# Optimization experiments

Hardware: AMD Instinct MI355X
Metric: run time of the kernel (lower is better)

Reference implementation:

```python
import jax, jax.numpy as jnp
import numpy as np

N = 20000          # nodes
E = 320000         # edges (avg degree 16)
MUL = 64           # multiplicity of 0e and 1o in hidden irreps
NUM_BASIS = 8
HID = 64           # radial MLP hidden
NSPEC = 4          # node attribute (species) scalars
N_NEIGH = 16.0
SILU_NORM = 1.679177  # e3nn normalize2mom constant for silu


def silu_n(x):
    return jax.nn.silu(x) * SILU_NORM


def setup_inputs() -> dict:
    key = jax.random.key(0)
    ks = jax.random.split(key, 20)
    inp = {
        'node_scalars': jax.random.normal(ks[0], (N, MUL), jnp.float32),
        'node_vectors': jax.random.normal(ks[1], (N, MUL, 3), jnp.float32),
        'node_attr': jax.random.uniform(ks[2], (N, NSPEC), jnp.float32),
        'edge_sh': jax.random.normal(ks[3], (E, 4), jnp.float32),
        'edge_embedded': jax.random.uniform(ks[4], (E, NUM_BASIS), jnp.float32),
        'edge_src': jax.random.randint(ks[5], (E,), 0, N),
        'edge_dst': jax.random.randint(ks[6], (E,), 0, N),
        # e3nn Linear #1 (64x0e+64x1o -> same)
        'W_lin1_s': jax.random.normal(ks[7], (MUL, MUL), jnp.float32),
        'W_lin1_v': jax.random.normal(ks[8], (MUL, MUL), jnp.float32),
        # radial FullyConnectedNet 8 -> 64 -> 64 -> 256
        'W_fc0': jax.random.normal(ks[9], (NUM_BASIS, HID), jnp.float32),
        'W_fc1': jax.random.normal(ks[10], (HID, HID), jnp.float32),
        'W_fc2': jax.random.normal(ks[11], (HID, 4 * MUL), jnp.float32),
        # e3nn Linear #2 (128x0e+128x1o -> 128x0e+64x1o)
        'W_lin2_s': jax.random.normal(ks[12], (2 * MUL, 2 * MUL), jnp.float32),
        'W_lin2_v': jax.random.normal(ks[13], (2 * MUL, MUL), jnp.float32),
        # self-connection FullyConnectedTensorProduct weights
        'W_sc_s': jax.random.normal(ks[14], (MUL, NSPEC, 2 * MUL), jnp.float32),
        'W_sc_v': jax.random.normal(ks[15], (MUL, NSPEC, MUL), jnp.float32),
    }
    return inp


def reference(node_scalars, node_vectors, node_attr, edge_sh, edge_embedded,
              W_lin1_s, W_lin1_v, W_fc0, W_fc1, W_fc2, W_lin2_s, W_lin2_v,
              W_sc_s, W_sc_v, edge_src, edge_dst):
    inv_sqrt3 = 1.0 / jnp.sqrt(jnp.float32(3.0))
    # ---- self connection (FullyConnectedTensorProduct with scalar attrs) ----
    sc_norm = 1.0 / jnp.sqrt(jnp.float32(MUL * NSPEC))
    sc_s = jnp.einsum('nu,nv,uvw->nw', node_scalars, node_attr, W_sc_s) * sc_norm   # [N,128]
    sc_v = jnp.einsum('nui,nv,uvw->nwi', node_vectors, node_attr, W_sc_v) * sc_norm  # [N,64,3]
    # ---- e3nn Linear #1 ----
    lin_norm = 1.0 / jnp.sqrt(jnp.float32(MUL))
    s = (node_scalars @ W_lin1_s) * lin_norm                      # [N,64]
    v = jnp.einsum('nui,uw->nwi', node_vectors, W_lin1_v) * lin_norm  # [N,64,3]
    # ---- gather to edges ----
    s_e = s[edge_src]          # [E,64]
    v_e = v[edge_src]          # [E,64,3]
    y0 = edge_sh[:, :1]        # [E,1]  (0e)
    y1 = edge_sh[:, 1:4]       # [E,3]  (1o)
    # ---- radial MLP -> per-edge TP weights ----
    h = silu_n((edge_embedded @ W_fc0) / jnp.sqrt(jnp.float32(NUM_BASIS)))
    h = silu_n((h @ W_fc1) / jnp.sqrt(jnp.float32(HID)))
    w = (h @ W_fc2) / jnp.sqrt(jnp.float32(HID))                  # [E,256]
    wA, wB, wC, wD = w[:, :MUL], w[:, MUL:2*MUL], w[:, 2*MUL:3*MUL], w[:, 3*MUL:]
    # ---- per-edge CG tensor product ('uvu', component normalization) ----
    oA = wA * s_e * y0                                            # 0e x 0e -> 0e  [E,64]
    oD = wD * jnp.einsum('eui,ei->eu', v_e, y1) * inv_sqrt3       # 1o x 1o -> 0e  [E,64]
    oB = wB[:, :, None] * s_e[:, :, None] * y1[:, None, :]        # 0e x 1o -> 1o  [E,64,3]
    oC = wC[:, :, None] * v_e * y0[:, :, None]                    # 1o x 0e -> 1o  [E,64,3]
    # ---- scatter-sum to destination nodes, normalize by neighbors ----
    s_agg = jax.ops.segment_sum(jnp.concatenate([oA, oD], axis=-1), edge_dst, num_segments=N) / N_NEIGH  # [N,128]
    v_agg = jax.ops.segment_sum(jnp.concatenate([oB, oC], axis=1), edge_dst, num_segments=N) / N_NEIGH   # [N,128,3]
    # ---- e3nn Linear #2 (128x0e+128x1o -> 128x0e+64x1o) ----
    lin2_norm = 1.0 / jnp.sqrt(jnp.float32(2 * MUL))
    s_h = (s_agg @ W_lin2_s) * lin2_norm                          # [N,128]
    v_h = jnp.einsum('nui,uw->nwi', v_agg, W_lin2_v) * lin2_norm  # [N,64,3]
    # ---- self connection ----
    s_h = s_h + sc_s
    v_h = v_h + sc_v
    # ---- Gate (even irreps -> normalized silu) ----
    out_s = silu_n(s_h[:, :MUL])                                  # scalars [N,64]
    out_v = silu_n(s_h[:, MUL:])[:, :, None] * v_h                # gated vectors [N,64,3]
    return jnp.concatenate([out_s, out_v.reshape(out_v.shape[0], MUL * 3)], axis=-1)  # [N,256]
```

## Files before the change

### kernel.cpp

```cpp
#include <hip/hip_runtime.h>
#include <math.h>

#define N_NODES 20000
#define N_EDGES 320000
#define MUL 64
#define NUM_BASIS 8
#define HID 64
#define NSPEC 4

#define LIN_NORM     0.125f
#define INV_SQRT8    0.3535533906f
#define LIN2_NORM    0.08838834765f
#define SC_NORM      0.0625f
#define INV_NEIGH    0.0625f
#define INV_SQRT3    0.5773502692f
#define SILU_NORM    1.679177f

typedef __attribute__((ext_vector_type(8))) short bf16x8;
typedef __attribute__((ext_vector_type(4))) float f32x4;

__device__ __forceinline__ float silu_n(float x) {
    float s = 1.0f / (1.0f + __expf(-x));
    return x * s * SILU_NORM;
}

__device__ __forceinline__ float bcast(float x, int l) {
    return __uint_as_float(__builtin_amdgcn_readlane(__float_as_uint(x), l));
}
__device__ __forceinline__ int bcast_i(int x, int l) {
    return __builtin_amdgcn_readlane(x, l);
}

__device__ __forceinline__ unsigned short f2bf(float x) {
    unsigned int u = __float_as_uint(x);
    unsigned int r = (u + 0x7fffu + ((u >> 16) & 1u)) >> 16;
    return (unsigned short)r;
}

__device__ __forceinline__ unsigned int cvtpk(float lo, float hi) {
    unsigned int r;
    asm("v_cvt_pk_bf16_f32 %0, %1, %2" : "=v"(r) : "v"(lo), "v"(hi));
    return r;
}

__device__ __forceinline__ bf16x8 cvt8(float f0, float f1, float f2, float f3,
                                       float f4, float f5, float f6, float f7) {
    union { unsigned int u[4]; bf16x8 v; } r;
    r.u[0] = cvtpk(f0, f1);
    r.u[1] = cvtpk(f2, f3);
    r.u[2] = cvtpk(f4, f5);
    r.u[3] = cvtpk(f6, f7);
    return r.v;
}

__global__ __launch_bounds__(256) void k_hist(const int* __restrict__ edst,
                                              int* __restrict__ counts)
{
    int e = blockIdx.x * blockDim.x + threadIdx.x;
    if (e < N_EDGES) atomicAdd(&counts[edst[e]], 1);
}

#define SCAN_T 1024
__global__ __launch_bounds__(SCAN_T) void k_scan(const int* __restrict__ counts,
                                                 int* __restrict__ cursor)
{
    __shared__ int part[SCAN_T];
    int t = threadIdx.x;
    const int CH = (N_NODES + SCAN_T - 1) / SCAN_T;
    int b0 = t * CH;
    int s = 0;
    for (int i = 0; i < CH; ++i) {
        int idx = b0 + i;
        if (idx < N_NODES) s += counts[idx];
    }
    part[t] = s;
    __syncthreads();
    for (int off = 1; off < SCAN_T; off <<= 1) {
        int v = (t >= off) ? part[t - off] : 0;
        __syncthreads();
        part[t] += v;
        __syncthreads();
    }
    int run = (t == 0) ? 0 : part[t - 1];
    for (int i = 0; i < CH; ++i) {
        int idx = b0 + i;
        if (idx < N_NODES) {
            cursor[idx] = run;
            run += counts[idx];
        }
    }
}

__global__ __launch_bounds__(256) void k_fill(const int* __restrict__ edst,
                                              const int* __restrict__ esrc,
                                              const float* __restrict__ sh,
                                              const float* __restrict__ emb,
                                              int* __restrict__ cursor,
                                              int* __restrict__ dlist,
                                              int* __restrict__ slist,
                                              float4* __restrict__ ysort,
                                              float4* __restrict__ esort)
{
    int e = blockIdx.x * blockDim.x + threadIdx.x;
    if (e < N_EDGES) {
        int d = edst[e];
        int pos = atomicAdd(&cursor[d], 1);
        dlist[pos] = d;
        slist[pos] = esrc[e];
        ysort[pos] = ((const float4*)sh)[e];
        esort[(size_t)pos * 2]     = ((const float4*)emb)[(size_t)e * 2];
        esort[(size_t)pos * 2 + 1] = ((const float4*)emb)[(size_t)e * 2 + 1];
    }
}

__global__ __launch_bounds__(256) void k_wprep(
    const float* __restrict__ W1, const float* __restrict__ W2,
    const float* __restrict__ Wl2s, const float* __restrict__ Wl2v,
    const float* __restrict__ Wscs, const float* __restrict__ Wscv,
    const float* __restrict__ W0,
    const float* __restrict__ Wl1s, const float* __restrict__ Wl1v,
    unsigned short* __restrict__ w1f, unsigned short* __restrict__ w2f,
    unsigned short* __restrict__ bsf, unsigned short* __restrict__ bvf,
    unsigned short* __restrict__ w0f,
    unsigned short* __restrict__ l1sf, unsigned short* __restrict__ l1vf)
{
    int t = blockIdx.x * 256 + threadIdx.x;
    if (t < 512) {
        int f = t >> 6, lane = t & 63;
        int kt = f >> 2, nt = f & 3, q = lane >> 4, c = lane & 15;
        #pragma unroll
        for (int j = 0; j < 8; ++j) {
            int k = kt * 32 + q * 8 + j;
            int n = nt * 16 + c;
            w1f[(size_t)t * 8 + j] = f2bf(W1[k * 64 + n]);
        }
    } else if (t < 2560) {
        int tt = t - 512;
        int f = tt >> 6, lane = tt & 63;
        int kt = f >> 4, nt = f & 15, q = lane >> 4, c = lane & 15;
        #pragma unroll
        for (int j = 0; j < 8; ++j) {
            int k = kt * 32 + q * 8 + j;
            int n = nt * 16 + c;
            w2f[(size_t)tt * 8 + j] = f2bf(W2[k * 256 + n]);
        }
    } else if (t < 4608) {
        int tt = t - 2560;
        int f = tt >> 6, lane = tt & 63;
        int kt = f >> 3, nt = f & 7, q = lane >> 4, c = lane & 15;
        #pragma unroll
        for (int j = 0; j < 8; ++j) {
            int k = kt * 32 + q * 8 + j;
            int n = nt * 16 + c;
            bsf[(size_t)tt * 8 + j] = f2bf(Wl2s[k * 128 + n] * LIN2_NORM);
        }
    } else if (t < 8704) {
        int tt = t - 4608;
        int f = tt >> 6, lane = tt & 63;
        int v = f >> 4, g = f & 15;
        int kt = g >> 3, nt = g & 7, q = lane >> 4, c = lane & 15;
        #pragma unroll
        for (int j = 0; j < 8; ++j) {
            int u = kt * 32 + q * 8 + j;
            int n = nt * 16 + c;
            bsf[(size_t)(2048 + tt) * 8 + j] = f2bf(Wscs[(u * 4 + v) * 128 + n] * SC_NORM);
        }
    } else if (t < 9728) {
        int tt = t - 8704;
        int f = tt >> 6, lane = tt & 63;
        int kt = f >> 2, nt = f & 3, q = lane >> 4, c = lane & 15;
        #pragma unroll
        for (int j = 0; j < 8; ++j) {
            int k = kt * 32 + q * 8 + j;
            int n = nt * 16 + c;
            bvf[(size_t)tt * 8 + j] = f2bf(Wl2v[k * 64 + n] * LIN2_NORM);
        }
    } else if (t < 11776) {
        int tt = t - 9728;
        int f = tt >> 6, lane = tt & 63;
        int v = f >> 3, g = f & 7;
        int kt = g >> 2, nt = g & 3, q = lane >> 4, c = lane & 15;
        #pragma unroll
        for (int j = 0; j < 8; ++j) {
            int u = kt * 32 + q * 8 + j;
            int n = nt * 16 + c;
            bvf[(size_t)(1024 + tt) * 8 + j] = f2bf(Wscv[(u * 4 + v) * 64 + n] * SC_NORM);
        }
    } else if (t < 12032) {
        int tt = t - 11776;
        int f = tt >> 6, lane = tt & 63;
        int q = lane >> 4, c = lane & 15;
        #pragma unroll
        for (int j = 0; j < 8; ++j) {
            int k = q * 8 + j;
            int n = f * 16 + c;
            w0f[(size_t)tt * 8 + j] =
                (k < 8) ? f2bf(W0[k * 64 + n] * INV_SQRT8) : (unsigned short)0;
        }
    } else if (t < 12544) {
        int tt = t - 12032;
        int f = tt >> 6, lane = tt & 63;
        int kt = f >> 2, nt = f & 3, q = lane >> 4, c = lane & 15;
        #pragma unroll
        for (int j = 0; j < 8; ++j) {
            int k = kt * 32 + q * 8 + j;
            int n = nt * 16 + c;
            l1sf[(size_t)tt * 8 + j] = f2bf(Wl1s[k * 64 + n] * LIN_NORM);
        }
    } else if (t < 13056) {
        int tt = t - 12544;
        int f = tt >> 6, lane = tt & 63;
        int kt = f >> 2, nt = f & 3, q = lane >> 4, c = lane & 15;
        #pragma unroll
        for (int j = 0; j < 8; ++j) {
            int k = kt * 32 + q * 8 + j;
            int n = nt * 16 + c;
            l1vf[(size_t)tt * 8 + j] = f2bf(Wl1v[k * 64 + n] * LIN_NORM);
        }
    }
}

__global__ __launch_bounds__(256) void k_node_lin1(
    const float* __restrict__ ns, const float* __restrict__ nv,
    const unsigned short* __restrict__ l1sf, const unsigned short* __restrict__ l1vf,
    float* __restrict__ s_out, float* __restrict__ v_out)
{
    const size_t NV = (size_t)N_NODES * 64;
    int lane = threadIdx.x & 63;
    int wtile = (blockIdx.x * blockDim.x + threadIdx.x) >> 6;
    int n0 = __builtin_amdgcn_readfirstlane(wtile * 16);
    if (n0 >= N_NODES) return;
    int q = lane >> 4, c = lane & 15;
    int node = n0 + c;

    f32x4 Ds[4];
    #pragma unroll
    for (int nt = 0; nt < 4; ++nt) Ds[nt] = (f32x4){0.f, 0.f, 0.f, 0.f};
    #pragma unroll
    for (int kt = 0; kt < 2; ++kt) {
        const float* ap = ns + (size_t)node * 64 + kt * 32 + q * 8;
        float4 a0 = *(const float4*)ap;
        float4 a1 = *(const float4*)(ap + 4);
        bf16x8 A = cvt8(a0.x, a0.y, a0.z, a0.w, a1.x, a1.y, a1.z, a1.w);
        #pragma unroll
        for (int nt = 0; nt < 4; ++nt) {
            bf16x8 B = *(const bf16x8*)(l1sf + (size_t)((kt * 4 + nt) * 64 + lane) * 8);
            Ds[nt] = __builtin_amdgcn_mfma_f32_16x16x32_bf16(A, B, Ds[nt], 0, 0, 0);
        }
    }
    #pragma unroll
    for (int nt = 0; nt < 4; ++nt)
        #pragma unroll
        for (int r = 0; r < 4; ++r)
            s_out[(size_t)(n0 + q * 4 + r) * 64 + nt * 16 + c] = Ds[nt][r];

    #pragma unroll 1
    for (int p = 0; p < 3; ++p) {
        f32x4 Dv[4];
        #pragma unroll
        for (int nt = 0; nt < 4; ++nt) Dv[nt] = (f32x4){0.f, 0.f, 0.f, 0.f};
        #pragma unroll
        for (int kt = 0; kt < 2; ++kt) {
            float f[8];
            #pragma unroll
            for (int j = 0; j < 8; ++j)
                f[j] = nv[(size_t)node * 192 + (size_t)(kt * 32 + q * 8 + j) * 3 + p];
            bf16x8 A = cvt8(f[0], f[1], f[2], f[3], f[4], f[5], f[6], f[7]);
            #pragma unroll
            for (int nt = 0; nt < 4; ++nt) {
                bf16x8 B = *(const bf16x8*)(l1vf + (size_t)((kt * 4 + nt) * 64 + lane) * 8);
                Dv[nt] = __builtin_amdgcn_mfma_f32_16x16x32_bf16(A, B, Dv[nt], 0, 0, 0);
            }
        }
        #pragma unroll
        for (int nt = 0; nt < 4; ++nt)
            #pragma unroll
            for (int r = 0; r < 4; ++r)
                v_out[p * NV + (size_t)(n0 + q * 4 + r) * 64 + nt * 16 + c] = Dv[nt][r];
    }
}

__global__ __launch_bounds__(256) void k_edge_fused(
    const float* __restrict__ esort,
    const unsigned short* __restrict__ w0f,
    const unsigned short* __restrict__ w1f, const unsigned short* __restrict__ w2f,
    const int* __restrict__ slist, const int* __restrict__ dlist,
    const float* __restrict__ ysort,
    const float* __restrict__ s_in, const float* __restrict__ v_in,
    float* __restrict__ s_agg, float* __restrict__ v_agg)
{
    const size_t NP2 = (size_t)N_NODES * 128;
    const size_t NV  = (size_t)N_NODES * 64;

    __shared__ unsigned short h0t[4 * 16 * 72];
    __shared__ unsigned short h1t[4 * 16 * 72];
    __shared__ unsigned int   wl1[4 * 16 * 66];
    __shared__ unsigned int   wl2[4 * 16 * 66];

    int lane = threadIdx.x & 63;
    int wid  = threadIdx.x >> 6;
    int q = lane >> 4;
    int c = lane & 15;
    int lbase = __builtin_amdgcn_readfirstlane(blockIdx.x * 256 + wid * 64);
    unsigned short* myh0 = h0t + wid * (16 * 72);
    unsigned short* myh1 = h1t + wid * (16 * 72);
    unsigned int*   myw1 = wl1 + wid * (16 * 66);
    unsigned int*   myw2 = wl2 + wid * (16 * 66);

    int srcv = slist[lbase + lane];
    int dstv = dlist[lbase + lane];
    float4 y4 = ((const float4*)ysort)[lbase + lane];

    bf16x8 B0[4];
    #pragma unroll
    for (int f = 0; f < 4; ++f)
        B0[f] = *(const bf16x8*)(w0f + (size_t)(f * 64 + lane) * 8);
    bf16x8 B1[2][4];
    #pragma unroll
    for (int f = 0; f < 8; ++f)
        B1[f >> 2][f & 3] = *(const bf16x8*)(w1f + (size_t)(f * 64 + lane) * 8);

    const float4* e4 = (const float4*)esort;
    const float WS  = 0.125f * INV_NEIGH;
    const float WSD = WS * INV_SQRT3;

    float accA = 0.f, aB0 = 0.f, aB1 = 0.f, aB2 = 0.f;
    float accD = 0.f, aC0 = 0.f, aC1 = 0.f, aC2 = 0.f;
    int cur = bcast_i(dstv, 0);

    #pragma unroll 1
    for (int mt = 0; mt < 4; ++mt) {
        int tb16 = mt * 16;

        float4 ea = {0.f, 0.f, 0.f, 0.f}, eb = {0.f, 0.f, 0.f, 0.f};
        if (q == 0) {
            ea = e4[(size_t)(lbase + tb16 + c) * 2];
            eb = e4[(size_t)(lbase + tb16 + c) * 2 + 1];
        }
        bf16x8 Ae = cvt8(ea.x, ea.y, ea.z, ea.w, eb.x, eb.y, eb.z, eb.w);
        f32x4 D0[4];
        #pragma unroll
        for (int nt = 0; nt < 4; ++nt) {
            f32x4 z = {0.f, 0.f, 0.f, 0.f};
            D0[nt] = __builtin_amdgcn_mfma_f32_16x16x32_bf16(Ae, B0[nt], z, 0, 0, 0);
        }
        #pragma unroll
        for (int nt = 0; nt < 4; ++nt)
            #pragma unroll
            for (int r = 0; r < 4; ++r)
                myh0[(q * 4 + r) * 72 + nt * 16 + c] = f2bf(silu_n(D0[nt][r]));
        __builtin_amdgcn_s_waitcnt(0xC07F);
        bf16x8 A0[2];
        #pragma unroll
        for (int kt = 0; kt < 2; ++kt)
            A0[kt] = *(const bf16x8*)(myh0 + c * 72 + kt * 32 + q * 8);

        f32x4 D1[4];
        #pragma unroll
        for (int nt = 0; nt < 4; ++nt) {
            f32x4 z = {0.f, 0.f, 0.f, 0.f};
            D1[nt] = __builtin_amdgcn_mfma_f32_16x16x32_bf16(A0[0], B1[0][nt], z, 0, 0, 0);
            D1[nt] = __builtin_amdgcn_mfma_f32_16x16x32_bf16(A0[1], B1[1][nt], D1[nt], 0, 0, 0);
        }
        #pragma unroll
        for (int nt = 0; nt < 4; ++nt)
            #pragma unroll
            for (int r = 0; r < 4; ++r)
                myh1[(q * 4 + r) * 72 + nt * 16 + c] = f2bf(silu_n(D1[nt][r] * 0.125f));
        __builtin_amdgcn_s_waitcnt(0xC07F);
        bf16x8 A1[2];
        #pragma unroll
        for (int kt = 0; kt < 2; ++kt)
            A1[kt] = *(const bf16x8*)(myh1 + c * 72 + kt * 32 + q * 8);

        #pragma unroll
        for (int half = 0; half < 2; ++half) {
            int ga = half * 2, gb = half * 2 + 1;
            f32x4 Da[4], Db[4];
            #pragma unroll
            for (int ntl = 0; ntl < 4; ++ntl) {
                bf16x8 b0 = *(const bf16x8*)(w2f + (size_t)((ga * 4 + ntl) * 64 + lane) * 8);
                bf16x8 b1 = *(const bf16x8*)(w2f + (size_t)((16 + ga * 4 + ntl) * 64 + lane) * 8);
                f32x4 z = {0.f, 0.f, 0.f, 0.f};
                Da[ntl] = __builtin_amdgcn_mfma_f32_16x16x32_bf16(A1[0], b0, z, 0, 0, 0);
                Da[ntl] = __builtin_amdgcn_mfma_f32_16x16x32_bf16(A1[1], b1, Da[ntl], 0, 0, 0);
            }
            #pragma unroll
            for (int ntl = 0; ntl < 4; ++ntl) {
                bf16x8 b0 = *(const bf16x8*)(w2f + (size_t)((gb * 4 + ntl) * 64 + lane) * 8);
                bf16x8 b1 = *(const bf16x8*)(w2f + (size_t)((16 + gb * 4 + ntl) * 64 + lane) * 8);
                f32x4 z = {0.f, 0.f, 0.f, 0.f};
                Db[ntl] = __builtin_amdgcn_mfma_f32_16x16x32_bf16(A1[0], b0, z, 0, 0, 0);
                Db[ntl] = __builtin_amdgcn_mfma_f32_16x16x32_bf16(A1[1], b1, Db[ntl], 0, 0, 0);
            }
            float sb = half ? WSD : WS;
            unsigned int* pp = half ? myw2 : myw1;
            #pragma unroll
            for (int ntl = 0; ntl < 4; ++ntl)
                #pragma unroll
                for (int r = 0; r < 4; ++r)
                    pp[(q * 4 + r) * 66 + ntl * 16 + c] = cvtpk(Da[ntl][r] * WS, Db[ntl][r] * sb);
        }
        __builtin_amdgcn_s_waitcnt(0xC07F);

        #pragma unroll 1
        for (int ebl = 0; ebl < 16; ebl += 8) {
            float se8[8], v08[8], v18[8], v28[8];
            unsigned int wab[8], wcd[8];
            #pragma unroll
            for (int i = 0; i < 8; ++i) {
                int et = ebl + i;
                int src = bcast_i(srcv, tb16 + et);
                wab[i] = myw1[et * 66 + lane];
                wcd[i] = myw2[et * 66 + lane];
                se8[i] = s_in[(size_t)src * 64 + lane];
                v08[i] = v_in[0 * NV + (size_t)src * 64 + lane];
                v18[i] = v_in[1 * NV + (size_t)src * 64 + lane];
                v28[i] = v_in[2 * NV + (size_t)src * 64 + lane];
            }
            #pragma unroll
            for (int i = 0; i < 8; ++i) {
                int e = tb16 + ebl + i;
                int dst = bcast_i(dstv, e);
                float y0 = bcast(y4.x, e), yx = bcast(y4.y, e);
                float yy = bcast(y4.z, e), yz = bcast(y4.w, e);
                if (dst != cur) {
                    size_t db = (size_t)cur * 128;
                    unsafeAtomicAdd(&s_agg[db + lane], accA);
                    unsafeAtomicAdd(&s_agg[db + 64 + lane], accD);
                    unsafeAtomicAdd(&v_agg[0 * NP2 + db + lane], aB0);
                    unsafeAtomicAdd(&v_agg[1 * NP2 + db + lane], aB1);
                    unsafeAtomicAdd(&v_agg[2 * NP2 + db + lane], aB2);
                    unsafeAtomicAdd(&v_agg[0 * NP2 + db + 64 + lane], aC0);
                    unsafeAtomicAdd(&v_agg[1 * NP2 + db + 64 + lane], aC1);
                    unsafeAtomicAdd(&v_agg[2 * NP2 + db + 64 + lane], aC2);
                    accA = aB0 = aB1 = aB2 = 0.f;
                    accD = aC0 = aC1 = aC2 = 0.f;
                    cur = dst;
                }
                float wA = __uint_as_float(wab[i] << 16);
                float wB = __uint_as_float(wab[i] & 0xffff0000u);
                float wC = __uint_as_float(wcd[i] << 16);
                float wD = __uint_as_float(wcd[i] & 0xffff0000u);
                accA = fmaf(wA, se8[i] * y0, accA);
                float bB = wB * se8[i];
                aB0 = fmaf(bB, yx, aB0);
                aB1 = fmaf(bB, yy, aB1);
                aB2 = fmaf(bB, yz, aB2);
                float dot = v08[i] * yx + v18[i] * yy + v28[i] * yz;
                accD = fmaf(wD, dot, accD);
                float bC = wC * y0;
                aC0 = fmaf(bC, v08[i], aC0);
                aC1 = fmaf(bC, v18[i], aC1);
                aC2 = fmaf(bC, v28[i], aC2);
            }
        }
    }
    {
        size_t db = (size_t)cur * 128;
        unsafeAtomicAdd(&s_agg[db + lane], accA);
        unsafeAtomicAdd(&s_agg[db + 64 + lane], accD);
        unsafeAtomicAdd(&v_agg[0 * NP2 + db + lane], aB0);
        unsafeAtomicAdd(&v_agg[1 * NP2 + db + lane], aB1);
        unsafeAtomicAdd(&v_agg[2 * NP2 + db + lane], aB2);
        unsafeAtomicAdd(&v_agg[0 * NP2 + db + 64 + lane], aC0);
        unsafeAtomicAdd(&v_agg[1 * NP2 + db + 64 + lane], aC1);
        unsafeAtomicAdd(&v_agg[2 * NP2 + db + 64 + lane], aC2);
    }
}

__global__ __launch_bounds__(256) void k_node_out_mfma(
    const float* __restrict__ ns, const float* __restrict__ nv,
    const float* __restrict__ na,
    const unsigned short* __restrict__ bsf, const unsigned short* __restrict__ bvf,
    const float* __restrict__ s_agg, const float* __restrict__ v_agg,
    float* __restrict__ out)
{
    const size_t NP2 = (size_t)N_NODES * 128;
    int lane = threadIdx.x & 63;
    int wtile = (blockIdx.x * blockDim.x + threadIdx.x) >> 6;
    int n0 = __builtin_amdgcn_readfirstlane(wtile * 16);
    if (n0 >= N_NODES) return;
    int q = lane >> 4, c = lane & 15;
    int node = n0 + c;

    float pa[4];
    #pragma unroll
    for (int v = 0; v < 4; ++v) pa[v] = na[(size_t)node * 4 + v];

    f32x4 Ds[8];
    #pragma unroll
    for (int nt = 0; nt < 8; ++nt) Ds[nt] = (f32x4){0.f, 0.f, 0.f, 0.f};

    #pragma unroll
    for (int kt = 0; kt < 4; ++kt) {
        const float* ap = s_agg + (size_t)node * 128 + kt * 32 + q * 8;
        float4 a0 = *(const float4*)ap;
        float4 a1 = *(const float4*)(ap + 4);
        bf16x8 A;
        A[0] = (short)f2bf(a0.x); A[1] = (short)f2bf(a0.y);
        A[2] = (short)f2bf(a0.z); A[3] = (short)f2bf(a0.w);
        A[4] = (short)f2bf(a1.x); A[5] = (short)f2bf(a1.y);
        A[6] = (short)f2bf(a1.z); A[7] = (short)f2bf(a1.w);
        #pragma unroll
        for (int nt = 0; nt < 8; ++nt) {
            bf16x8 B = *(const bf16x8*)(bsf + (size_t)((kt * 8 + nt) * 64 + lane) * 8);
            Ds[nt] = __builtin_amdgcn_mfma_f32_16x16x32_bf16(A, B, Ds[nt], 0, 0, 0);
        }
    }
    {
        const float* np_ = ns + (size_t)node * 64 + q * 8;
        float4 n00 = *(const float4*)np_;
        float4 n01 = *(const float4*)(np_ + 4);
        float4 n10 = *(const float4*)(np_ + 32);
        float4 n11 = *(const float4*)(np_ + 36);
        float nsr[16] = {n00.x, n00.y, n00.z, n00.w, n01.x, n01.y, n01.z, n01.w,
                         n10.x, n10.y, n10.z, n10.w, n11.x, n11.y, n11.z, n11.w};
        #pragma unroll
        for (int v = 0; v < 4; ++v) {
            float sv = pa[v];
            #pragma unroll
            for (int kt = 0; kt < 2; ++kt) {
                bf16x8 A;
                #pragma unroll
                for (int j = 0; j < 8; ++j)
                    A[j] = (short)f2bf(nsr[kt * 8 + j] * sv);
                #pragma unroll
                for (int nt = 0; nt < 8; ++nt) {
                    bf16x8 B = *(const bf16x8*)(bsf +
                        (size_t)((32 + v * 16 + kt * 8 + nt) * 64 + lane) * 8);
                    Ds[nt] = __builtin_amdgcn_mfma_f32_16x16x32_bf16(A, B, Ds[nt], 0, 0, 0);
                }
            }
        }
    }
    float gs[4][4];
    #pragma unroll
    for (int nt = 0; nt < 4; ++nt)
        #pragma unroll
        for (int r = 0; r < 4; ++r) {
            out[(size_t)(n0 + q * 4 + r) * 256 + nt * 16 + c] = silu_n(Ds[nt][r]);
            gs[nt][r] = silu_n(Ds[4 + nt][r]);
        }

    #pragma unroll 1
    for (int p = 0; p < 3; ++p) {
        f32x4 Dv[4];
        #pragma unroll
        for (int nt = 0; nt < 4; ++nt) Dv[nt] = (f32x4){0.f, 0.f, 0.f, 0.f};

        #pragma unroll
        for (int kt = 0; kt < 4; ++kt) {
            const float* ap = v_agg + (size_t)p * NP2 + (size_t)node * 128 + kt * 32 + q * 8;
            float4 a0 = *(const float4*)ap;
            float4 a1 = *(const float4*)(ap + 4);
            bf16x8 A;
            A[0] = (short)f2bf(a0.x); A[1] = (short)f2bf(a0.y);
            A[2] = (short)f2bf(a0.z); A[3] = (short)f2bf(a0.w);
            A[4] = (short)f2bf(a1.x); A[5] = (short)f2bf(a1.y);
            A[6] = (short)f2bf(a1.z); A[7] = (short)f2bf(a1.w);
            #pragma unroll
            for (int nt = 0; nt < 4; ++nt) {
                bf16x8 B = *(const bf16x8*)(bvf + (size_t)((kt * 4 + nt) * 64 + lane) * 8);
                Dv[nt] = __builtin_amdgcn_mfma_f32_16x16x32_bf16(A, B, Dv[nt], 0, 0, 0);
            }
        }
        float nvr[16];
        #pragma unroll
        for (int j = 0; j < 8; ++j) {
            nvr[j]     = nv[(size_t)node * 192 + (size_t)(q * 8 + j) * 3 + p];
            nvr[8 + j] = nv[(size_t)node * 192 + (size_t)(32 + q * 8 + j) * 3 + p];
        }
        #pragma unroll
        for (int v = 0; v < 4; ++v) {
            float sv = pa[v];
            #pragma unroll
            for (int kt = 0; kt < 2; ++kt) {
                bf16x8 A;
                #pragma unroll
                for (int j = 0; j < 8; ++j)
                    A[j] = (short)f2bf(nvr[kt * 8 + j] * sv);
                #pragma unroll
                for (int nt = 0; nt < 4; ++nt) {
                    bf16x8 B = *(const bf16x8*)(bvf +
                        (size_t)((16 + v * 8 + kt * 4 + nt) * 64 + lane) * 8);
                    Dv[nt] = __builtin_amdgcn_mfma_f32_16x16x32_bf16(A, B, Dv[nt], 0, 0, 0);
                }
            }
        }
        #pragma unroll
        for (int nt = 0; nt < 4; ++nt)
            #pragma unroll
            for (int r = 0; r < 4; ++r) {
                int w = nt * 16 + c;
                out[(size_t)(n0 + q * 4 + r) * 256 + 64 + (size_t)w * 3 + p]
                    = gs[nt][r] * Dv[nt][r];
            }
    }
}

extern "C" void kernel_launch(void* const* d_in, const int* in_sizes, int n_in,
                              void* d_out, int out_size, void* d_ws, size_t ws_size,
                              hipStream_t stream)
{
    const float* node_scalars = (const float*)d_in[0];
    const float* node_vectors = (const float*)d_in[1];
    const float* node_attr    = (const float*)d_in[2];
    const float* edge_sh      = (const float*)d_in[3];
    const float* edge_emb     = (const float*)d_in[4];
    const int*   edge_src     = (const int*)d_in[5];
    const int*   edge_dst     = (const int*)d_in[6];
    const float* W_lin1_s = (const float*)d_in[7];
    const float* W_lin1_v = (const float*)d_in[8];
    const float* W_fc0    = (const float*)d_in[9];
    const float* W_fc1    = (const float*)d_in[10];
    const float* W_fc2    = (const float*)d_in[11];
    const float* W_lin2_s = (const float*)d_in[12];
    const float* W_lin2_v = (const float*)d_in[13];
    const float* W_sc_s   = (const float*)d_in[14];
    const float* W_sc_v   = (const float*)d_in[15];
    float* out = (float*)d_out;

    float* ws    = (float*)d_ws;
    float* s_agg = ws;
    float* v_agg = s_agg + (size_t)N_NODES * 128;
    float* s_buf = v_agg + 3 * (size_t)N_NODES * 128;
    float* v_buf = s_buf + (size_t)N_NODES * 64;
    int*   counts = (int*)(v_buf + 3 * (size_t)N_NODES * 64);
    int*   cursor = counts + N_NODES;
    int*   dlist  = cursor + N_NODES;
    int*   slist  = dlist + N_EDGES;
    unsigned short* w1f  = (unsigned short*)(slist + N_EDGES);
    unsigned short* w2f  = w1f + 4096;
    unsigned short* bsf  = w2f + 16384;
    unsigned short* bvf  = bsf + 49152;
    unsigned short* w0f  = bvf + 24576;
    unsigned short* l1sf = w0f + 2048;
    unsigned short* l1vf = l1sf + 4096;
    float4* ysort = (float4*)(l1vf + 4096);
    float4* esort = ysort + N_EDGES;

    hipMemsetAsync(counts, 0, (size_t)N_NODES * sizeof(int), stream);
    hipMemsetAsync(s_agg, 0, (size_t)N_NODES * 512 * sizeof(float), stream);

    {
        int blocks = (N_EDGES + 255) / 256;
        k_hist<<<blocks, 256, 0, stream>>>(edge_dst, counts);
        k_scan<<<1, SCAN_T, 0, stream>>>(counts, cursor);
        k_fill<<<blocks, 256, 0, stream>>>(edge_dst, edge_src, edge_sh, edge_emb,
                                           cursor, dlist, slist, ysort, esort);
    }
    k_wprep<<<51, 256, 0, stream>>>(W_fc1, W_fc2, W_lin2_s, W_lin2_v,
                                    W_sc_s, W_sc_v, W_fc0, W_lin1_s, W_lin1_v,
                                    w1f, w2f, bsf, bvf, w0f, l1sf, l1vf);
    {
        int blocks = (1250 + 3) / 4;
        k_node_lin1<<<blocks, 256, 0, stream>>>(node_scalars, node_vectors,
                                                l1sf, l1vf, s_buf, v_buf);
    }
    {
        int blocks = N_EDGES / 256;
        k_edge_fused<<<blocks, 256, 0, stream>>>((const float*)esort, w0f, w1f, w2f,
                                                 slist, dlist, (const float*)ysort,
                                                 s_buf, v_buf, s_agg, v_agg);
    }
    {
        int blocks = (1250 + 3) / 4;
        k_node_out_mfma<<<blocks, 256, 0, stream>>>(
            node_scalars, node_vectors, node_attr, bsf, bvf,
            s_agg, v_agg, out);
    }
}
```

Baseline: 343.9 us.

## Interleave lin1 vector output as float4 and split edge gather into two phases

The lin1 kernel now writes node vectors as one padded float4 per node/channel instead of three separate planes. The edge kernel then fetches a source vector with a single 16-byte load rather than three scalar loads. The edge kernel also merges its LDS buffers into one reused buffer and splits the final stage into two passes, each with its own running accumulators and atomic flushes. This is meant to cut LDS footprint and register pressure so occupancy can rise. The cost is a third more memory for the padded vectors and some repeated broadcast and destination checking across the two passes.

```diff
diff --git a/kernel.cpp b/kernel.cpp
--- a/kernel.cpp
+++ b/kernel.cpp
@@ -223,9 +223,8 @@
 __global__ __launch_bounds__(256) void k_node_lin1(
     const float* __restrict__ ns, const float* __restrict__ nv,
     const unsigned short* __restrict__ l1sf, const unsigned short* __restrict__ l1vf,
-    float* __restrict__ s_out, float* __restrict__ v_out)
-{
-    const size_t NV = (size_t)N_NODES * 64;
+    float* __restrict__ s_out, float4* __restrict__ v4_out)
+{
     int lane = threadIdx.x & 63;
     int wtile = (blockIdx.x * blockDim.x + threadIdx.x) >> 6;
     int n0 = __builtin_amdgcn_readfirstlane(wtile * 16);
@@ -254,11 +253,13 @@
         for (int r = 0; r < 4; ++r)
             s_out[(size_t)(n0 + q * 4 + r) * 64 + nt * 16 + c] = Ds[nt][r];
 
+    f32x4 Dv[3][4];
+    #pragma unroll
+    for (int p = 0; p < 3; ++p)
+        #pragma unroll
+        for (int nt = 0; nt < 4; ++nt) Dv[p][nt] = (f32x4){0.f, 0.f, 0.f, 0.f};
     #pragma unroll 1
     for (int p = 0; p < 3; ++p) {
-        f32x4 Dv[4];
-        #pragma unroll
-        for (int nt = 0; nt < 4; ++nt) Dv[nt] = (f32x4){0.f, 0.f, 0.f, 0.f};
         #pragma unroll
         for (int kt = 0; kt < 2; ++kt) {
             float f[8];
@@ -269,15 +270,17 @@
             #pragma unroll
             for (int nt = 0; nt < 4; ++nt) {
                 bf16x8 B = *(const bf16x8*)(l1vf + (size_t)((kt * 4 + nt) * 64 + lane) * 8);
-                Dv[nt] = __builtin_amdgcn_mfma_f32_16x16x32_bf16(A, B, Dv[nt], 0, 0, 0);
-            }
-        }
-        #pragma unroll
-        for (int nt = 0; nt < 4; ++nt)
-            #pragma unroll
-            for (int r = 0; r < 4; ++r)
-                v_out[p * NV + (size_t)(n0 + q * 4 + r) * 64 + nt * 16 + c] = Dv[nt][r];
-    }
+                Dv[p][nt] = __builtin_amdgcn_mfma_f32_16x16x32_bf16(A, B, Dv[p][nt], 0, 0, 0);
+            }
+        }
+    }
+    #pragma unroll
+    for (int nt = 0; nt < 4; ++nt)
+        #pragma unroll
+        for (int r = 0; r < 4; ++r) {
+            float4 vv = {Dv[0][nt][r], Dv[1][nt][r], Dv[2][nt][r], 0.f};
+            v4_out[(size_t)(n0 + q * 4 + r) * 64 + nt * 16 + c] = vv;
+        }
 }
 
 __global__ __launch_bounds__(256) void k_edge_fused(
@@ -286,26 +289,21 @@
     const unsigned short* __restrict__ w1f, const unsigned short* __restrict__ w2f,
     const int* __restrict__ slist, const int* __restrict__ dlist,
     const float* __restrict__ ysort,
-    const float* __restrict__ s_in, const float* __restrict__ v_in,
+    const float* __restrict__ s_in, const float4* __restrict__ v4_in,
     float* __restrict__ s_agg, float* __restrict__ v_agg)
 {
     const size_t NP2 = (size_t)N_NODES * 128;
-    const size_t NV  = (size_t)N_NODES * 64;
-
-    __shared__ unsigned short h0t[4 * 16 * 72];
-    __shared__ unsigned short h1t[4 * 16 * 72];
-    __shared__ unsigned int   wl1[4 * 16 * 66];
-    __shared__ unsigned int   wl2[4 * 16 * 66];
+
+    __shared__ unsigned short ht[4 * 16 * 72];
+    __shared__ unsigned int   wl[4 * 16 * 66];
 
     int lane = threadIdx.x & 63;
     int wid  = threadIdx.x >> 6;
     int q = lane >> 4;
     int c = lane & 15;
     int lbase = __builtin_amdgcn_readfirstlane(blockIdx.x * 256 + wid * 64);
-    unsigned short* myh0 = h0t + wid * (16 * 72);
-    unsigned short* myh1 = h1t + wid * (16 * 72);
-    unsigned int*   myw1 = wl1 + wid * (16 * 66);
-    unsigned int*   myw2 = wl2 + wid * (16 * 66);
+    unsigned short* myh = ht + wid * (16 * 72);
+    unsigned int*   myw = wl + wid * (16 * 66);
 
     int srcv = slist[lbase + lane];
     int dstv = dlist[lbase + lane];
@@ -326,7 +324,8 @@
 
     float accA = 0.f, aB0 = 0.f, aB1 = 0.f, aB2 = 0.f;
     float accD = 0.f, aC0 = 0.f, aC1 = 0.f, aC2 = 0.f;
-    int cur = bcast_i(dstv, 0);
+    int cur1 = bcast_i(dstv, 0);
+    int cur2 = cur1;
 
     #pragma unroll 1
     for (int mt = 0; mt < 4; ++mt) {
@@ -348,12 +347,12 @@
         for (int nt = 0; nt < 4; ++nt)
             #pragma unroll
             for (int r = 0; r < 4; ++r)
-                myh0[(q * 4 + r) * 72 + nt * 16 + c] = f2bf(silu_n(D0[nt][r]));
+                myh[(q * 4 + r) * 72 + nt * 16 + c] = f2bf(silu_n(D0[nt][r]));
         __builtin_amdgcn_s_waitcnt(0xC07F);
         bf16x8 A0[2];
         #pragma unroll
         for (int kt = 0; kt < 2; ++kt)
-            A0[kt] = *(const bf16x8*)(myh0 + c * 72 + kt * 32 + q * 8);
+            A0[kt] = *(const bf16x8*)(myh + c * 72 + kt * 32 + q * 8);
 
         f32x4 D1[4];
         #pragma unroll
@@ -366,14 +365,14 @@
         for (int nt = 0; nt < 4; ++nt)
             #pragma unroll
             for (int r = 0; r < 4; ++r)
-                myh1[(q * 4 + r) * 72 + nt * 16 + c] = f2bf(silu_n(D1[nt][r] * 0.125f));
+                myh[(q * 4 + r) * 72 + nt * 16 + c] = f2bf(silu_n(D1[nt][r] * 0.125f));
         __builtin_amdgcn_s_waitcnt(0xC07F);
         bf16x8 A1[2];
         #pragma unroll
         for (int kt = 0; kt < 2; ++kt)
-            A1[kt] = *(const bf16x8*)(myh1 + c * 72 + kt * 32 + q * 8);
-
-        #pragma unroll
+            A1[kt] = *(const bf16x8*)(myh + c * 72 + kt * 32 + q * 8);
+
+        #pragma unroll 1
         for (int half = 0; half < 2; ++half) {
             int ga = half * 2, gb = half * 2 + 1;
             f32x4 Da[4], Db[4];
@@ -394,75 +393,99 @@
                 Db[ntl] = __builtin_amdgcn_mfma_f32_16x16x32_bf16(A1[1], b1, Db[ntl], 0, 0, 0);
             }
             float sb = half ? WSD : WS;
-            unsigned int* pp = half ? myw2 : myw1;
             #pragma unroll
             for (int ntl = 0; ntl < 4; ++ntl)
                 #pragma unroll
                 for (int r = 0; r < 4; ++r)
-                    pp[(q * 4 + r) * 66 + ntl * 16 + c] = cvtpk(Da[ntl][r] * WS, Db[ntl][r] * sb);
-        }
-        __builtin_amdgcn_s_waitcnt(0xC07F);
-
-        #pragma unroll 1
-        for (int ebl = 0; ebl < 16; ebl += 8) {
-            float se8[8], v08[8], v18[8], v28[8];
-            unsigned int wab[8], wcd[8];
-            #pragma unroll
-            for (int i = 0; i < 8; ++i) {
-                int et = ebl + i;
-                int src = bcast_i(srcv, tb16 + et);
-                wab[i] = myw1[et * 66 + lane];
-                wcd[i] = myw2[et * 66 + lane];
-                se8[i] = s_in[(size_t)src * 64 + lane];
-                v08[i] = v_in[0 * NV + (size_t)src * 64 + lane];
-                v18[i] = v_in[1 * NV + (size_t)src * 64 + lane];
-                v28[i] = v_in[2 * NV + (size_t)src * 64 + lane];
-            }
-            #pragma unroll
-            for (int i = 0; i < 8; ++i) {
-                int e = tb16 + ebl + i;
-                int dst = bcast_i(dstv, e);
-                float y0 = bcast(y4.x, e), yx = bcast(y4.y, e);
-                float yy = bcast(y4.z, e), yz = bcast(y4.w, e);
-                if (dst != cur) {
-                    size_t db = (size_t)cur * 128;
-                    unsafeAtomicAdd(&s_agg[db + lane], accA);
-                    unsafeAtomicAdd(&s_agg[db + 64 + lane], accD);
-                    unsafeAtomicAdd(&v_agg[0 * NP2 + db + lane], aB0);
-                    unsafeAtomicAdd(&v_agg[1 * NP2 + db + lane], aB1);
-                    unsafeAtomicAdd(&v_agg[2 * NP2 + db + lane], aB2);
-                    unsafeAtomicAdd(&v_agg[0 * NP2 + db + 64 + lane], aC0);
-                    unsafeAtomicAdd(&v_agg[1 * NP2 + db + 64 + lane], aC1);
-                    unsafeAtomicAdd(&v_agg[2 * NP2 + db + 64 + lane], aC2);
-                    accA = aB0 = aB1 = aB2 = 0.f;
-                    accD = aC0 = aC1 = aC2 = 0.f;
-                    cur = dst;
+                    myw[(q * 4 + r) * 66 + ntl * 16 + c] = cvtpk(Da[ntl][r] * WS, Db[ntl][r] * sb);
+            __builtin_amdgcn_s_waitcnt(0xC07F);
+
+            if (half == 0) {
+                #pragma unroll 1
+                for (int ebl = 0; ebl < 16; ebl += 8) {
+                    float se8[8];
+                    unsigned int wab[8];
+                    #pragma unroll
+                    for (int i = 0; i < 8; ++i) {
+                        int et = ebl + i;
+                        int src = bcast_i(srcv, tb16 + et);
+                        wab[i] = myw[et * 66 + lane];
+                        se8[i] = s_in[(size_t)src * 64 + lane];
+                    }
+                    #pragma unroll
+                    for (int i = 0; i < 8; ++i) {
+                        int e = tb16 + ebl + i;
+                        int dst = bcast_i(dstv, e);
+                        float y0 = bcast(y4.x, e), yx = bcast(y4.y, e);
+                        float yy = bcast(y4.z, e), yz = bcast(y4.w, e);
+                        if (dst != cur1) {
+                            size_t db = (size_t)cur1 * 128;
+                            unsafeAtomicAdd(&s_agg[db + lane], accA);
+                            unsafeAtomicAdd(&v_agg[0 * NP2 + db + lane], aB0);
+                            unsafeAtomicAdd(&v_agg[1 * NP2 + db + lane], aB1);
+                            unsafeAtomicAdd(&v_agg[2 * NP2 + db + lane], aB2);
+                            accA = aB0 = aB1 = aB2 = 0.f;
+                            cur1 = dst;
+                        }
+                        float wA = __uint_as_float(wab[i] << 16);
+                        float wB = __uint_as_float(wab[i] & 0xffff0000u);
+                        accA = fmaf(wA, se8[i] * y0, accA);
+                        float bB = wB * se8[i];
+                        aB0 = fmaf(bB, yx, aB0);
+                        aB1 = fmaf(bB, yy, aB1);
+                        aB2 = fmaf(bB, yz, aB2);
+                    }
                 }
-                float wA = __uint_as_float(wab[i] << 16);
-                float wB = __uint_as_float(wab[i] & 0xffff0000u);
-                float wC = __uint_as_float(wcd[i] << 16);
-                float wD = __uint_as_float(wcd[i] & 0xffff0000u);
-                accA = fmaf(wA, se8[i] * y0, accA);
-                float bB = wB * se8[i];
-                aB0 = fmaf(bB, yx, aB0);
-                aB1 = fmaf(bB, yy, aB1);
-                aB2 = fmaf(bB, yz, aB2);
-                float dot = v08[i] * yx + v18[i] * yy + v28[i] * yz;
-                accD = fmaf(wD, dot, accD);
-                float bC = wC * y0;
-                aC0 = fmaf(bC, v08[i], aC0);
-                aC1 = fmaf(bC, v18[i], aC1);
-                aC2 = fmaf(bC, v28[i], aC2);
+            } else {
+                #pragma unroll 1
+                for (int ebl = 0; ebl < 16; ebl += 8) {
+                    float4 vv[8];
+                    unsigned int wcd[8];
+                    #pragma unroll
+                    for (int i = 0; i < 8; ++i) {
+                        int et = ebl + i;
+                        int src = bcast_i(srcv, tb16 + et);
+                        wcd[i] = myw[et * 66 + lane];
+                        vv[i] = v4_in[(size_t)src * 64 + lane];
+                    }
+                    #pragma unroll
+                    for (int i = 0; i < 8; ++i) {
+                        int e = tb16 + ebl + i;
+                        int dst = bcast_i(dstv, e);
+                        float y0 = bcast(y4.x, e), yx = bcast(y4.y, e);
+                        float yy = bcast(y4.z, e), yz = bcast(y4.w, e);
+                        if (dst != cur2) {
+                            size_t db = (size_t)cur2 * 128;
+                            unsafeAtomicAdd(&s_agg[db + 64 + lane], accD);
+                            unsafeAtomicAdd(&v_agg[0 * NP2 + db + 64 + lane], aC0);
+                            unsafeAtomicAdd(&v_agg[1 * NP2 + db + 64 + lane], aC1);
+                            unsafeAtomicAdd(&v_agg[2 * NP2 + db + 64 + lane], aC2);
+                            accD = aC0 = aC1 = aC2 = 0.f;
+                            cur2 = dst;
+                        }
+                        float wC = __uint_as_float(wcd[i] << 16);
+                        float wD = __uint_as_float(wcd[i] & 0xffff0000u);
+                        float dot = vv[i].x * yx + vv[i].y * yy + vv[i].z * yz;
+                        accD = fmaf(wD, dot, accD);
+                        float bC = wC * y0;
+                        aC0 = fmaf(bC, vv[i].x, aC0);
+                        aC1 = fmaf(bC, vv[i].y, aC1);
+                        aC2 = fmaf(bC, vv[i].z, aC2);
+                    }
+                }
             }
         }
     }
     {
-        size_t db = (size_t)cur * 128;
+        size_t db = (size_t)cur1 * 128;
         unsafeAtomicAdd(&s_agg[db + lane], accA);
-        unsafeAtomicAdd(&s_agg[db + 64 + lane], accD);
         unsafeAtomicAdd(&v_agg[0 * NP2 + db + lane], aB0);
         unsafeAtomicAdd(&v_agg[1 * NP2 + db + lane], aB1);
         unsafeAtomicAdd(&v_agg[2 * NP2 + db + lane], aB2);
+    }
+    {
+        size_t db = (size_t)cur2 * 128;
+        unsafeAtomicAdd(&s_agg[db + 64 + lane], accD);
         unsafeAtomicAdd(&v_agg[0 * NP2 + db + 64 + lane], aC0);
         unsafeAtomicAdd(&v_agg[1 * NP2 + db + 64 + lane], aC1);
         unsafeAtomicAdd(&v_agg[2 * NP2 + db + 64 + lane], aC2);
@@ -625,8 +648,8 @@
     float* s_agg = ws;
     float* v_agg = s_agg + (size_t)N_NODES * 128;
     float* s_buf = v_agg + 3 * (size_t)N_NODES * 128;
-    float* v_buf = s_buf + (size_t)N_NODES * 64;
-    int*   counts = (int*)(v_buf + 3 * (size_t)N_NODES * 64);
+    float4* v4_buf = (float4*)(s_buf + (size_t)N_NODES * 64);
+    int*   counts = (int*)(v4_buf + (size_t)N_NODES * 64);
     int*   cursor = counts + N_NODES;
     int*   dlist  = cursor + N_NODES;
     int*   slist  = dlist + N_EDGES;
@@ -656,13 +679,13 @@
     {
         int blocks = (1250 + 3) / 4;
         k_node_lin1<<<blocks, 256, 0, stream>>>(node_scalars, node_vectors,
-                                                l1sf, l1vf, s_buf, v_buf);
+                                                l1sf, l1vf, s_buf, v4_buf);
     }
     {
         int blocks = N_EDGES / 256;
         k_edge_fused<<<blocks, 256, 0, stream>>>((const float*)esort, w0f, w1f, w2f,
                                                  slist, dlist, (const float*)ysort,
-                                                 s_buf, v_buf, s_agg, v_agg);
+                                                 s_buf, v4_buf, s_agg, v_agg);
     }
     {
         int blocks = (1250 + 3) / 4;
```

Result: slower. 365.7 us (+6.3%).

## Split node kernels across more waves per node tile to raise parallelism

Applied to the files above, without the earlier changes.

The lin1 node kernel now gives each 16-node tile four waves: one for the scalar part and one for each vector component, instead of a single wave doing all four serially. The output kernel is split into a scalar kernel, which writes the gate activations to a new workspace buffer, and a vector kernel with one wave per (tile, component). The aim is more waves in flight for these small node kernels, which launched only about 313 blocks before. The cost is one extra kernel launch, an extra global round trip for the gate values, and reloading node attributes and weights once per component.

```diff
diff --git a/kernel.cpp b/kernel.cpp
--- a/kernel.cpp
+++ b/kernel.cpp
@@ -227,35 +227,36 @@
 {
     const size_t NV = (size_t)N_NODES * 64;
     int lane = threadIdx.x & 63;
-    int wtile = (blockIdx.x * blockDim.x + threadIdx.x) >> 6;
-    int n0 = __builtin_amdgcn_readfirstlane(wtile * 16);
+    int gwave = (blockIdx.x * blockDim.x + threadIdx.x) >> 6;
+    int part = __builtin_amdgcn_readfirstlane(gwave & 3);
+    int n0 = __builtin_amdgcn_readfirstlane((gwave >> 2) * 16);
     if (n0 >= N_NODES) return;
     int q = lane >> 4, c = lane & 15;
     int node = n0 + c;
 
-    f32x4 Ds[4];
-    #pragma unroll
-    for (int nt = 0; nt < 4; ++nt) Ds[nt] = (f32x4){0.f, 0.f, 0.f, 0.f};
-    #pragma unroll
-    for (int kt = 0; kt < 2; ++kt) {
-        const float* ap = ns + (size_t)node * 64 + kt * 32 + q * 8;
-        float4 a0 = *(const float4*)ap;
-        float4 a1 = *(const float4*)(ap + 4);
-        bf16x8 A = cvt8(a0.x, a0.y, a0.z, a0.w, a1.x, a1.y, a1.z, a1.w);
-        #pragma unroll
-        for (int nt = 0; nt < 4; ++nt) {
-            bf16x8 B = *(const bf16x8*)(l1sf + (size_t)((kt * 4 + nt) * 64 + lane) * 8);
-            Ds[nt] = __builtin_amdgcn_mfma_f32_16x16x32_bf16(A, B, Ds[nt], 0, 0, 0);
-        }
-    }
-    #pragma unroll
-    for (int nt = 0; nt < 4; ++nt)
-        #pragma unroll
-        for (int r = 0; r < 4; ++r)
-            s_out[(size_t)(n0 + q * 4 + r) * 64 + nt * 16 + c] = Ds[nt][r];
-
-    #pragma unroll 1
-    for (int p = 0; p < 3; ++p) {
+    if (part == 0) {
+        f32x4 Ds[4];
+        #pragma unroll
+        for (int nt = 0; nt < 4; ++nt) Ds[nt] = (f32x4){0.f, 0.f, 0.f, 0.f};
+        #pragma unroll
+        for (int kt = 0; kt < 2; ++kt) {
+            const float* ap = ns + (size_t)node * 64 + kt * 32 + q * 8;
+            float4 a0 = *(const float4*)ap;
+            float4 a1 = *(const float4*)(ap + 4);
+            bf16x8 A = cvt8(a0.x, a0.y, a0.z, a0.w, a1.x, a1.y, a1.z, a1.w);
+            #pragma unroll
+            for (int nt = 0; nt < 4; ++nt) {
+                bf16x8 B = *(const bf16x8*)(l1sf + (size_t)((kt * 4 + nt) * 64 + lane) * 8);
+                Ds[nt] = __builtin_amdgcn_mfma_f32_16x16x32_bf16(A, B, Ds[nt], 0, 0, 0);
+            }
+        }
+        #pragma unroll
+        for (int nt = 0; nt < 4; ++nt)
+            #pragma unroll
+            for (int r = 0; r < 4; ++r)
+                s_out[(size_t)(n0 + q * 4 + r) * 64 + nt * 16 + c] = Ds[nt][r];
+    } else {
+        int p = part - 1;
         f32x4 Dv[4];
         #pragma unroll
         for (int nt = 0; nt < 4; ++nt) Dv[nt] = (f32x4){0.f, 0.f, 0.f, 0.f};
@@ -469,14 +470,12 @@
     }
 }
 
-__global__ __launch_bounds__(256) void k_node_out_mfma(
-    const float* __restrict__ ns, const float* __restrict__ nv,
-    const float* __restrict__ na,
-    const unsigned short* __restrict__ bsf, const unsigned short* __restrict__ bvf,
-    const float* __restrict__ s_agg, const float* __restrict__ v_agg,
-    float* __restrict__ out)
-{
-    const size_t NP2 = (size_t)N_NODES * 128;
+__global__ __launch_bounds__(256) void k_node_out_s(
+    const float* __restrict__ ns, const float* __restrict__ na,
+    const unsigned short* __restrict__ bsf,
+    const float* __restrict__ s_agg,
+    float* __restrict__ out, float* __restrict__ gbuf)
+{
     int lane = threadIdx.x & 63;
     int wtile = (blockIdx.x * blockDim.x + threadIdx.x) >> 6;
     int n0 = __builtin_amdgcn_readfirstlane(wtile * 16);
@@ -534,69 +533,85 @@
             }
         }
     }
-    float gs[4][4];
     #pragma unroll
     for (int nt = 0; nt < 4; ++nt)
         #pragma unroll
         for (int r = 0; r < 4; ++r) {
             out[(size_t)(n0 + q * 4 + r) * 256 + nt * 16 + c] = silu_n(Ds[nt][r]);
-            gs[nt][r] = silu_n(Ds[4 + nt][r]);
-        }
-
-    #pragma unroll 1
-    for (int p = 0; p < 3; ++p) {
-        f32x4 Dv[4];
-        #pragma unroll
-        for (int nt = 0; nt < 4; ++nt) Dv[nt] = (f32x4){0.f, 0.f, 0.f, 0.f};
-
-        #pragma unroll
-        for (int kt = 0; kt < 4; ++kt) {
-            const float* ap = v_agg + (size_t)p * NP2 + (size_t)node * 128 + kt * 32 + q * 8;
-            float4 a0 = *(const float4*)ap;
-            float4 a1 = *(const float4*)(ap + 4);
+            gbuf[(size_t)(n0 + q * 4 + r) * 64 + nt * 16 + c] = silu_n(Ds[4 + nt][r]);
+        }
+}
+
+__global__ __launch_bounds__(256) void k_node_out_v(
+    const float* __restrict__ nv, const float* __restrict__ na,
+    const unsigned short* __restrict__ bvf,
+    const float* __restrict__ v_agg, const float* __restrict__ gbuf,
+    float* __restrict__ out)
+{
+    const size_t NP2 = (size_t)N_NODES * 128;
+    int lane = threadIdx.x & 63;
+    int gwave = (blockIdx.x * blockDim.x + threadIdx.x) >> 6;
+    if (gwave >= 3750) return;
+    int p = __builtin_amdgcn_readfirstlane(gwave % 3);
+    int n0 = __builtin_amdgcn_readfirstlane((gwave / 3) * 16);
+    int q = lane >> 4, c = lane & 15;
+    int node = n0 + c;
+
+    float pa[4];
+    #pragma unroll
+    for (int v = 0; v < 4; ++v) pa[v] = na[(size_t)node * 4 + v];
+
+    f32x4 Dv[4];
+    #pragma unroll
+    for (int nt = 0; nt < 4; ++nt) Dv[nt] = (f32x4){0.f, 0.f, 0.f, 0.f};
+
+    #pragma unroll
+    for (int kt = 0; kt < 4; ++kt) {
+        const float* ap = v_agg + (size_t)p * NP2 + (size_t)node * 128 + kt * 32 + q * 8;
+        float4 a0 = *(const float4*)ap;
+        float4 a1 = *(const float4*)(ap + 4);
+        bf16x8 A;
+        A[0] = (short)f2bf(a0.x); A[1] = (short)f2bf(a0.y);
+        A[2] = (short)f2bf(a0.z); A[3] = (short)f2bf(a0.w);
+        A[4] = (short)f2bf(a1.x); A[5] = (short)f2bf(a1.y);
+        A[6] = (short)f2bf(a1.z); A[7] = (short)f2bf(a1.w);
+        #pragma unroll
+        for (int nt = 0; nt < 4; ++nt) {
+            bf16x8 B = *(const bf16x8*)(bvf + (size_t)((kt * 4 + nt) * 64 + lane) * 8);
+            Dv[nt] = __builtin_amdgcn_mfma_f32_16x16x32_bf16(A, B, Dv[nt], 0, 0, 0);
+        }
+    }
+    float nvr[16];
+    #pragma unroll
+    for (int j = 0; j < 8; ++j) {
+        nvr[j]     = nv[(size_t)node * 192 + (size_t)(q * 8 + j) * 3 + p];
+        nvr[8 + j] = nv[(size_t)node * 192 + (size_t)(32 + q * 8 + j) * 3 + p];
+    }
+    #pragma unroll
+    for (int v = 0; v < 4; ++v) {
+        float sv = pa[v];
+        #pragma unroll
+        for (int kt = 0; kt < 2; ++kt) {
             bf16x8 A;
-            A[0] = (short)f2bf(a0.x); A[1] = (short)f2bf(a0.y);
-            A[2] = (short)f2bf(a0.z); A[3] = (short)f2bf(a0.w);
-            A[4] = (short)f2bf(a1.x); A[5] = (short)f2bf(a1.y);
-            A[6] = (short)f2bf(a1.z); A[7] = (short)f2bf(a1.w);
+            #pragma unroll
+            for (int j = 0; j < 8; ++j)
+                A[j] = (short)f2bf(nvr[kt * 8 + j] * sv);
             #pragma unroll
             for (int nt = 0; nt < 4; ++nt) {
-                bf16x8 B = *(const bf16x8*)(bvf + (size_t)((kt * 4 + nt) * 64 + lane) * 8);
+                bf16x8 B = *(const bf16x8*)(bvf +
+                    (size_t)((16 + v * 8 + kt * 4 + nt) * 64 + lane) * 8);
                 Dv[nt] = __builtin_amdgcn_mfma_f32_16x16x32_bf16(A, B, Dv[nt], 0, 0, 0);
             }
         }
-        float nvr[16];
-        #pragma unroll
-        for (int j = 0; j < 8; ++j) {
-            nvr[j]     = nv[(size_t)node * 192 + (size_t)(q * 8 + j) * 3 + p];
-            nvr[8 + j] = nv[(size_t)node * 192 + (size_t)(32 + q * 8 + j) * 3 + p];
-        }
-        #pragma unroll
-        for (int v = 0; v < 4; ++v) {
-            float sv = pa[v];
-            #pragma unroll
-            for (int kt = 0; kt < 2; ++kt) {
-                bf16x8 A;
-                #pragma unroll
-                for (int j = 0; j < 8; ++j)
-                    A[j] = (short)f2bf(nvr[kt * 8 + j] * sv);
-                #pragma unroll
-                for (int nt = 0; nt < 4; ++nt) {
-                    bf16x8 B = *(const bf16x8*)(bvf +
-                        (size_t)((16 + v * 8 + kt * 4 + nt) * 64 + lane) * 8);
-                    Dv[nt] = __builtin_amdgcn_mfma_f32_16x16x32_bf16(A, B, Dv[nt], 0, 0, 0);
-                }
-            }
-        }
-        #pragma unroll
-        for (int nt = 0; nt < 4; ++nt)
-            #pragma unroll
-            for (int r = 0; r < 4; ++r) {
-                int w = nt * 16 + c;
-                out[(size_t)(n0 + q * 4 + r) * 256 + 64 + (size_t)w * 3 + p]
-                    = gs[nt][r] * Dv[nt][r];
-            }
-    }
+    }
+    #pragma unroll
+    for (int nt = 0; nt < 4; ++nt)
+        #pragma unroll
+        for (int r = 0; r < 4; ++r) {
+            int w = nt * 16 + c;
+            float g = gbuf[(size_t)(n0 + q * 4 + r) * 64 + w];
+            out[(size_t)(n0 + q * 4 + r) * 256 + 64 + (size_t)w * 3 + p] = g * Dv[nt][r];
+        }
 }
 
 extern "C" void kernel_launch(void* const* d_in, const int* in_sizes, int n_in,
@@ -626,7 +641,8 @@
     float* v_agg = s_agg + (size_t)N_NODES * 128;
     float* s_buf = v_agg + 3 * (size_t)N_NODES * 128;
     float* v_buf = s_buf + (size_t)N_NODES * 64;
-    int*   counts = (int*)(v_buf + 3 * (size_t)N_NODES * 64);
+    float* gbuf  = v_buf + 3 * (size_t)N_NODES * 64;
+    int*   counts = (int*)(gbuf + (size_t)N_NODES * 64);
     int*   cursor = counts + N_NODES;
     int*   dlist  = cursor + N_NODES;
     int*   slist  = dlist + N_EDGES;
@@ -654,9 +670,8 @@
                                     W_sc_s, W_sc_v, W_fc0, W_lin1_s, W_lin1_v,
                                     w1f, w2f, bsf, bvf, w0f, l1sf, l1vf);
     {
-        int blocks = (1250 + 3) / 4;
-        k_node_lin1<<<blocks, 256, 0, stream>>>(node_scalars, node_vectors,
-                                                l1sf, l1vf, s_buf, v_buf);
+        k_node_lin1<<<1250, 256, 0, stream>>>(node_scalars, node_vectors,
+                                              l1sf, l1vf, s_buf, v_buf);
     }
     {
         int blocks = N_EDGES / 256;
@@ -666,8 +681,12 @@
     }
     {
         int blocks = (1250 + 3) / 4;
-        k_node_out_mfma<<<blocks, 256, 0, stream>>>(
-            node_scalars, node_vectors, node_attr, bsf, bvf,
-            s_agg, v_agg, out);
-    }
-}
+        k_node_out_s<<<blocks, 256, 0, stream>>>(node_scalars, node_attr, bsf,
+                                                 s_agg, out, gbuf);
+    }
+    {
+        int blocks = (3750 + 3) / 4;
+        k_node_out_v<<<blocks, 256, 0, stream>>>(node_vectors, node_attr, bvf,
+                                                 v_agg, gbuf, out);
+    }
+}
```

New measurement: 322.2 us. 6.3% less time.
